# Kernel tuning notes

Hardware: AMD Instinct MI355X
Metric: run time of the kernel (lower is better)

The kernel has to match this reference:

```python
import jax, jax.numpy as jnp
import numpy as np

ROPE_BASE = 10000.0

def rope_tables(n, r):
    inv = 1.0 / (ROPE_BASE ** (jnp.arange(0, r, 2, dtype=jnp.float32) / r))  # [r/2]
    ang = jnp.arange(n, dtype=jnp.float32)[:, None] * inv[None, :]           # [n, r/2]
    cos = jnp.concatenate([jnp.cos(ang), jnp.cos(ang)], axis=-1)             # [n, r]
    sin = jnp.concatenate([jnp.sin(ang), jnp.sin(ang)], axis=-1)
    return cos, sin

def apply_rope(x, cos, sin):
    # x: [B, H, T, r]; cos/sin: [T, r]
    half = x.shape[-1] // 2
    x_rot = jnp.concatenate([-x[..., half:], x[..., :half]], axis=-1)
    return x * cos + x_rot * sin

def setup_inputs() -> dict:
    key = jax.random.key(0)
    ks = jax.random.split(key, 8)
    B, S, L = 2, 1024, 1024
    dim_q, h, k, d_c, d_cq, r = 2048, 16, 128, 512, 1536, 64
    w = 0.02  # weight scale to keep activations numerically tame
    return {
        'hidden_q': jax.random.normal(ks[0], (B, S, dim_q), jnp.float32),
        'kv_c':     jax.random.normal(ks[1], (B, L, d_c), jnp.float32),
        'Wq':       jax.random.normal(ks[2], (h * k, dim_q), jnp.float32) * w,
        'w_kc_q':   jax.random.normal(ks[3], (h, k, d_cq), jnp.float32) * w,
        'W_qr':     jax.random.normal(ks[4], (h, d_cq, r), jnp.float32) * (w / np.sqrt(r)),
        'W_kr':     jax.random.normal(ks[5], (h, d_c, r), jnp.float32) * w,
        'w_kc_kv':  jax.random.normal(ks[6], (h, k, d_c), jnp.float32) * w,
        'Wo':       jax.random.normal(ks[7], (dim_q, h * k), jnp.float32) * w,
    }

def reference(hidden_q, kv_c, Wq, w_kc_q, W_qr, W_kr, w_kc_kv, Wo):
    B, S, _ = hidden_q.shape
    L = kv_c.shape[1]
    h, k, _ = w_kc_q.shape
    r = W_qr.shape[-1]
    # q projection: [B,S,h,k]
    q_hk = (hidden_q @ Wq.T).reshape(B, S, h, k)
    # low-rank expand to q-compressed space then retrieval space
    q_big = jnp.einsum('bshk,hkq->bshq', q_hk, w_kc_q)          # [B,S,h,d_cq]
    q_r = jnp.einsum('bshq,hqr->bhsr', q_big, W_qr)             # [B,h,S,r]
    k_r = jnp.einsum('bld,hdr->bhlr', kv_c, W_kr)               # [B,h,L,r]
    cos_S, sin_S = rope_tables(S, r)
    cos_L, sin_L = rope_tables(L, r)
    q_r = apply_rope(q_r, cos_S, sin_S)
    k_r = apply_rope(k_r, cos_L, sin_L)
    # attention in retrieval space, values are compressed kv (shared across heads)
    scores = jnp.einsum('bhsr,bhlr->bhsl', q_r, k_r)            # scale baked into W_qr
    attn = jax.nn.softmax(scores, axis=-1)
    ctx_c = jnp.einsum('bhsl,bld->bhsd', attn, kv_c)            # [B,h,S,d_c]
    # decompress per head: w_kc_kv is [h,k,d_c]
    ctx_lat = jnp.einsum('bhsd,hkd->bshk', ctx_c, w_kc_kv).reshape(B, S, h * k)
    return ctx_lat @ Wo.T
```

## Files before the change

kernel.cpp:

```cpp
#include <hip/hip_runtime.h>
#include <math.h>
#include <stdint.h>


typedef __attribute__((ext_vector_type(8))) short short8;
typedef __attribute__((ext_vector_type(4))) float f32x4;

#define GLOAD16(gsrc, ldst)                                                            \
  __builtin_amdgcn_global_load_lds((const __attribute__((address_space(1))) void*)(gsrc), \
                                   (__attribute__((address_space(3))) void*)(ldst), 16, 0, 0)

__device__ inline uint16_t f2b(float x) {
  uint32_t u = __builtin_bit_cast(uint32_t, x);
  u += 0x7fff + ((u >> 16) & 1);
  return (uint16_t)(u >> 16);
}
__device__ inline float b2f(uint16_t b) {
  uint32_t u = ((uint32_t)b) << 16;
  return __builtin_bit_cast(float, u);
}
__device__ inline uint32_t cvtpk_bf16(float lo, float hi) {
  uint32_t d;
  asm("v_cvt_pk_bf16_f32 %0, %1, %2" : "=v"(d) : "v"(lo), "v"(hi));
  return d;
}

__global__ __launch_bounds__(256) void convert5_kernel(
    const float* __restrict__ s0, uint16_t* __restrict__ t0, const float* __restrict__ s1,
    uint16_t* __restrict__ t1, const float* __restrict__ s2, uint16_t* __restrict__ t2,
    const float* __restrict__ s3, uint16_t* __restrict__ t3, const float* __restrict__ s4,
    uint16_t* __restrict__ t4) {
  int bid = blockIdx.x;
  const float* s;
  uint16_t* t;
  int off;
  if (bid < 2048) { s = s0; t = t0; off = bid; }
  else if (bid < 2560) { s = s1; t = t1; off = bid - 2048; }
  else if (bid < 3072) { s = s2; t = t2; off = bid - 2560; }
  else if (bid < 5120) { s = s3; t = t3; off = bid - 3072; }
  else { s = s4; t = t4; off = bid - 5120; }
  int i = off * 256 + threadIdx.x;
  const float4* s4v = (const float4*)s;
  float4 a = s4v[i * 2], b = s4v[i * 2 + 1];
  union {
    uint16_t u[8];
    uint4 v;
  } o;
  o.u[0] = f2b(a.x); o.u[1] = f2b(a.y); o.u[2] = f2b(a.z); o.u[3] = f2b(a.w);
  o.u[4] = f2b(b.x); o.u[5] = f2b(b.y); o.u[6] = f2b(b.z); o.u[7] = f2b(b.w);
  ((uint4*)t)[i] = o.v;
}

__global__ __launch_bounds__(256) void transpose_conv_kernel(const float* __restrict__ src,
                                                             uint16_t* __restrict__ dst,
                                                             int R, int C, int sOff, int dOff) {
  __shared__ float t[32][33];
  src += (size_t)blockIdx.z * sOff;
  dst += (size_t)blockIdx.z * dOff;
  int r0 = blockIdx.x * 32, c0 = blockIdx.y * 32;
  int tr = threadIdx.x >> 5, tc = threadIdx.x & 31;
#pragma unroll
  for (int i = 0; i < 4; ++i) t[tr + i * 8][tc] = src[(size_t)(r0 + tr + i * 8) * C + c0 + tc];
  __syncthreads();
#pragma unroll
  for (int i = 0; i < 4; ++i)
    dst[(size_t)(c0 + tr + i * 8) * R + r0 + tc] = f2b(t[tc][tr + i * 8]);
}

__global__ __launch_bounds__(64) void rope_tables_kernel(float* __restrict__ cosK,
                                                         float* __restrict__ sinK,
                                                         float* __restrict__ cosQ,
                                                         float* __restrict__ sinQ) {
  const float LOG2E = 1.44269504088896341f;
  int s = blockIdx.x;
  int j = threadIdx.x;
  int i = j & 31;
  float inv = powf(10000.0f, -(float)(2 * i) / 64.0f);
  float ang = (float)s * inv;
  float c = cosf(ang), sn = sinf(ang);
  cosK[s * 64 + j] = c;
  sinK[s * 64 + j] = sn;
  cosQ[s * 64 + j] = c * LOG2E;
  sinQ[s * 64 + j] = sn * LOG2E;
}

template <int BM, int EPI, int SPLITK = 1>
__global__ __launch_bounds__(256) void gemm_mfma_kernel(const uint16_t* __restrict__ A,
                                                        const uint16_t* __restrict__ Bt,
                                                        void* __restrict__ Cv, int K, int lda,
                                                        int ldb, int ldc, int aZ, int bZ, int cZ,
                                                        const float* __restrict__ rc,
                                                        const float* __restrict__ rs) {
  constexpr int MT = BM / 32;
  __shared__ __align__(16) uint16_t As[2][BM * 64];
  __shared__ __align__(16) uint16_t Bs[2][128 * 64];
  int z = blockIdx.z;
  if (SPLITK > 1) {
    int zh = z / SPLITK, zk = z % SPLITK;
    A += (size_t)zh * aZ + (size_t)zk * K;
    Bt += (size_t)zh * bZ + (size_t)zk * K;
  } else {
    A += (size_t)z * aZ;
    Bt += (size_t)z * bZ;
  }
  int m0 = blockIdx.x * BM, n0 = blockIdx.y * 128;
  int tid = threadIdx.x;
  int wave = tid >> 6, lane = tid & 63;
  int wm = wave >> 1, wn = wave & 1;
  int rS = lane >> 3, sl = lane & 7;
  int lr = lane >> 4, lc = lane & 15;

  auto stage = [&](int k0, int buf) {
#pragma unroll
    for (int i = 0; i < MT; ++i) {
      int idx = wave * MT + i;
      int row = idx * 8 + rS;
      GLOAD16(A + (size_t)(m0 + row) * lda + k0 + ((sl ^ (row & 7)) << 3),
              (uint8_t*)As[buf] + idx * 1024);
    }
#pragma unroll
    for (int i = 0; i < 4; ++i) {
      int idx = wave * 4 + i;
      int row = idx * 8 + rS;
      GLOAD16(Bt + (size_t)(n0 + row) * ldb + k0 + ((sl ^ (row & 7)) << 3),
              (uint8_t*)Bs[buf] + idx * 1024);
    }
  };

  f32x4 acc[MT][4] = {};
  stage(0, 0);
  int cur = 0;
  for (int k0 = 0; k0 < K; k0 += 64) {
    __syncthreads();
    if (k0 + 64 < K) stage(k0 + 64, cur ^ 1);
    short8 af[MT][2], bf[4][2];
#pragma unroll
    for (int t = 0; t < MT; ++t)
#pragma unroll
      for (int ks = 0; ks < 2; ++ks) {
        int slot = ks * 4 + lr;
        int ra = wm * (BM / 2) + t * 16 + lc;
        af[t][ks] =
            *(const short8*)((const uint8_t*)As[cur] + ra * 128 + ((slot ^ (ra & 7)) << 4));
      }
#pragma unroll
    for (int t = 0; t < 4; ++t)
#pragma unroll
      for (int ks = 0; ks < 2; ++ks) {
        int slot = ks * 4 + lr;
        int rb = wn * 64 + t * 16 + lc;
        bf[t][ks] =
            *(const short8*)((const uint8_t*)Bs[cur] + rb * 128 + ((slot ^ (rb & 7)) << 4));
      }
    __builtin_amdgcn_s_setprio(1);
#pragma unroll
    for (int mt = 0; mt < MT; ++mt)
#pragma unroll
      for (int nt = 0; nt < 4; ++nt) {
        acc[mt][nt] =
            __builtin_amdgcn_mfma_f32_16x16x32_bf16(af[mt][0], bf[nt][0], acc[mt][nt], 0, 0, 0);
        acc[mt][nt] =
            __builtin_amdgcn_mfma_f32_16x16x32_bf16(af[mt][1], bf[nt][1], acc[mt][nt], 0, 0, 0);
      }
    __builtin_amdgcn_s_setprio(0);
    cur ^= 1;
  }
  if (EPI == 3) {
#pragma unroll
    for (int mt = 0; mt < MT; ++mt)
#pragma unroll
      for (int nt = 0; nt < 4; ++nt)
#pragma unroll
        for (int r = 0; r < 4; ++r) {
          int m = m0 + wm * (BM / 2) + mt * 16 + lr * 4 + r;
          int n = n0 + wn * 64 + nt * 16 + lc;
          int pos = m & 1023, j = n & 63;
          float x = acc[mt][nt][r];
          float prt = acc[mt][nt ^ 2][r];
          float rot = (nt & 2) ? prt : -prt;
          float v = fmaf(x, rc[pos * 64 + j], rot * rs[pos * 64 + j]);
          ((uint16_t*)Cv)[(size_t)m * ldc + n] = f2b(v);
        }
  } else {
#pragma unroll
    for (int mt = 0; mt < MT; ++mt)
#pragma unroll
      for (int nt = 0; nt < 4; ++nt)
#pragma unroll
        for (int r = 0; r < 4; ++r) {
          int m = m0 + wm * (BM / 2) + mt * 16 + lr * 4 + r;
          int n = n0 + wn * 64 + nt * 16 + lc;
          float v = acc[mt][nt][r];
          if (EPI == 0)
            ((float*)Cv)[(size_t)z * cZ + (size_t)m * ldc + n] = v;
          else if (EPI == 1)
            ((uint16_t*)Cv)[(size_t)z * cZ + (size_t)m * ldc + n] = f2b(v);
          else
            ((uint16_t*)Cv)[((size_t)((m >> 10) * 2048 + n)) * 1024 + (m & 1023)] = f2b(v);
        }
  }
}

__global__ __launch_bounds__(256) void reduce1_kernel(const float* __restrict__ tp,
                                                      uint16_t* __restrict__ tmpT) {
  int gid = blockIdx.x * 256 + threadIdx.x;
  int zh = gid >> 13, e = gid & 8191;
  const float* b = tp + (size_t)zh * 32768 + e;
  tmpT[gid] = f2b(b[0] + b[8192] + b[16384] + b[24576]);
}

__global__ __launch_bounds__(512, 4) void flash3_kernel(const uint16_t* __restrict__ qrb,
                                                        const uint16_t* __restrict__ krb,
                                                        const uint16_t* __restrict__ VhT,
                                                        uint16_t* __restrict__ ctxlatb) {
  __shared__ __align__(16) uint8_t lds[67584];
  int bh = blockIdx.x;
  int b = bh >> 4, h = bh & 15;
  int s0 = blockIdx.y * 64;
  int tid = threadIdx.x, wave = tid >> 6, lane = tid & 63;
  int ig = wave >> 2, w = wave & 3;
  int lr = lane >> 4, lc = lane & 15;
  int rS = lane >> 3, sl = lane & 7;

  uint8_t* Ks = lds + ig * 8192;
  uint8_t* Vs = lds + 16384 + ig * 16384;
  uint8_t* Ps = lds + 49152 + wave * 2304;

  const uint16_t* qrow = qrb + (size_t)(b * 1024 + s0 + w * 16 + lc) * 1024 + h * 64;
  short8 qa[2];
  qa[0] = *(const short8*)(qrow + lr * 8);
  qa[1] = *(const short8*)(qrow + 32 + lr * 8);

  float m_run = -1e30f, l_run = 0.f;
  f32x4 o[8] = {};

  uint8_t* psW = Ps + lc * 144 + lr * 8;
  const uint8_t* psR = Ps + lc * 144 + lr * 16;

  const uint16_t* krbase = krb + (size_t)(b * 1024) * 1024 + h * 64;
  const uint16_t* vtbase = VhT + (size_t)(b * 2048 + h * 128) * 1024;

  auto stageKV = [&](int l0) {
#pragma unroll
    for (int i = 0; i < 2; ++i) {
      int idx = w * 2 + i;
      int row = idx * 8 + rS;
      GLOAD16(krbase + (size_t)(l0 + row) * 1024 + ((sl ^ (row & 7)) << 3), Ks + idx * 1024);
    }
#pragma unroll
    for (int i = 0; i < 4; ++i) {
      int idx = w * 4 + i;
      int row = idx * 8 + rS;
      GLOAD16(vtbase + (size_t)row * 1024 + l0 + ((sl ^ (row & 7)) << 3), Vs + idx * 1024);
    }
  };

  for (int t = 0; t < 8; ++t) {
    int l0 = ig * 512 + t * 64;
    __syncthreads();
    stageKV(l0);
    __syncthreads();

    f32x4 sc[4];
    __builtin_amdgcn_s_setprio(1);
#pragma unroll
    for (int nt = 0; nt < 4; ++nt) {
      int rowk = nt * 16 + lc;
      short8 kb0 = *(const short8*)(Ks + rowk * 128 + ((lr ^ (rowk & 7)) << 4));
      short8 kb1 = *(const short8*)(Ks + rowk * 128 + (((4 + lr) ^ (rowk & 7)) << 4));
      f32x4 z = {};
      z = __builtin_amdgcn_mfma_f32_16x16x32_bf16(kb0, qa[0], z, 0, 0, 0);
      sc[nt] = __builtin_amdgcn_mfma_f32_16x16x32_bf16(kb1, qa[1], z, 0, 0, 0);
    }
    __builtin_amdgcn_s_setprio(0);

    float mx = fmaxf(fmaxf(fmaxf(sc[0][0], sc[0][1]), fmaxf(sc[0][2], sc[0][3])),
                     fmaxf(fmaxf(sc[1][0], sc[1][1]), fmaxf(sc[1][2], sc[1][3])));
    float mx2 = fmaxf(fmaxf(fmaxf(sc[2][0], sc[2][1]), fmaxf(sc[2][2], sc[2][3])),
                      fmaxf(fmaxf(sc[3][0], sc[3][1]), fmaxf(sc[3][2], sc[3][3])));
    mx = fmaxf(mx, mx2);
    mx = fmaxf(mx, __shfl_xor(mx, 16));
    mx = fmaxf(mx, __shfl_xor(mx, 32));

    bool grow = mx > m_run + 8.0f;
    bool upd = (__ballot(grow) != 0ULL);
    float scale;
    if (upd) {
      float mn = fmaxf(m_run, mx);
      scale = exp2f(m_run - mn);
      m_run = mn;
    }

    float ps = 0.f;
#pragma unroll
    for (int nt = 0; nt < 4; ++nt) {
#pragma unroll
      for (int rp = 0; rp < 2; ++rp) {
        float p0 = exp2f(sc[nt][rp * 2] - m_run);
        float p1 = exp2f(sc[nt][rp * 2 + 1] - m_run);
        ps += p0 + p1;
        *(uint32_t*)(psW + nt * 32 + rp * 4) = cvtpk_bf16(p0, p1);
      }
    }
    ps += __shfl_xor(ps, 16);
    ps += __shfl_xor(ps, 32);

    if (upd) {
      l_run = l_run * scale + ps;
      float sc0 = __shfl(scale, lr * 4 + 0);
      float sc1 = __shfl(scale, lr * 4 + 1);
      float sc2 = __shfl(scale, lr * 4 + 2);
      float sc3 = __shfl(scale, lr * 4 + 3);
#pragma unroll
      for (int nt = 0; nt < 8; ++nt) {
        o[nt][0] *= sc0;
        o[nt][1] *= sc1;
        o[nt][2] *= sc2;
        o[nt][3] *= sc3;
      }
    } else {
      l_run += ps;
    }

    short8 pa[2];
    pa[0] = *(const short8*)(psR);
    pa[1] = *(const short8*)(psR + 64);
    __builtin_amdgcn_s_setprio(1);
#pragma unroll
    for (int nt = 0; nt < 8; ++nt) {
      int rowv = nt * 16 + lc;
      short8 vb0 = *(const short8*)(Vs + rowv * 128 + ((lr ^ (rowv & 7)) << 4));
      short8 vb1 = *(const short8*)(Vs + rowv * 128 + (((4 + lr) ^ (rowv & 7)) << 4));
      o[nt] = __builtin_amdgcn_mfma_f32_16x16x32_bf16(pa[0], vb0, o[nt], 0, 0, 0);
      o[nt] = __builtin_amdgcn_mfma_f32_16x16x32_bf16(pa[1], vb1, o[nt], 0, 0, 0);
    }
    __builtin_amdgcn_s_setprio(0);
  }

  __syncthreads();
  float2* mlx = (float2*)(lds + 49152);
  if (lr == 0) mlx[(ig * 4 + w) * 16 + lc] = make_float2(m_run, l_run);
  __syncthreads();
  float2 e0 = mlx[(0 * 4 + w) * 16 + lc];
  float2 e1 = mlx[(1 * 4 + w) * 16 + lc];
  float M = fmaxf(e0.x, e1.x);
  float a0 = exp2f(e0.x - M), a1 = exp2f(e1.x - M);
  float dinv = 1.0f / (e0.y * a0 + e1.y * a1);
  float myA = ig ? a1 : a0;
  float ar[4], dr[4];
#pragma unroll
  for (int r = 0; r < 4; ++r) {
    ar[r] = __shfl(myA, lr * 4 + r);
    dr[r] = __shfl(dinv, lr * 4 + r);
  }
  float* O1 = (float*)lds;
  int qb = w * 16 + lr * 4;
  if (ig == 1) {
#pragma unroll
    for (int nt = 0; nt < 8; ++nt)
#pragma unroll
      for (int r = 0; r < 4; ++r) O1[(qb + r) * 130 + nt * 16 + lc] = o[nt][r] * ar[r];
  }
  __syncthreads();
  if (ig == 0) {
    uint16_t* orow = ctxlatb + (size_t)(b * 1024 + s0 + w * 16) * 2048 + h * 128;
#pragma unroll
    for (int nt = 0; nt < 8; ++nt)
#pragma unroll
      for (int r = 0; r < 4; ++r) {
        float v = (o[nt][r] * ar[r] + O1[(qb + r) * 130 + nt * 16 + lc]) * dr[r];
        orow[(size_t)(lr * 4 + r) * 2048 + nt * 16 + lc] = f2b(v);
      }
  }
}

extern "C" void kernel_launch(void* const* d_in, const int* in_sizes, int n_in,
                              void* d_out, int out_size, void* d_ws, size_t ws_size,
                              hipStream_t stream) {
  const float* hidden_q = (const float*)d_in[0];
  const float* kv_c = (const float*)d_in[1];
  const float* Wq = (const float*)d_in[2];
  const float* w_kc_q = (const float*)d_in[3];
  const float* W_qr = (const float*)d_in[4];
  const float* W_kr = (const float*)d_in[5];
  const float* w_kc_kv = (const float*)d_in[6];
  const float* Wo = (const float*)d_in[7];
  float* out = (float*)d_out;

  const size_t MB = 1024 * 1024;
  uint8_t* base = (uint8_t*)d_ws;
  uint16_t* Wob = (uint16_t*)(base + 0 * MB);
  uint16_t* qrb = (uint16_t*)(base + 8 * MB);
  uint16_t* krb = (uint16_t*)(base + 12 * MB);
  uint16_t* VhT = (uint16_t*)(base + 16 * MB);
  uint16_t* ctxlatb = (uint16_t*)(base + 24 * MB);
  float* cosK = (float*)(base + 32 * MB);
  float* sinK = (float*)(base + 32 * MB + 262144);
  float* cosQ = (float*)(base + 32 * MB + 524288);
  float* sinQ = (float*)(base + 32 * MB + 786432);
  uint16_t* hqb = (uint16_t*)(base + 33 * MB);
  uint16_t* kvb = (uint16_t*)(base + 41 * MB);
  uint16_t* wkvb = (uint16_t*)(base + 43 * MB);
  uint16_t* WqT = (uint16_t*)(base + 45 * MB);
  uint16_t* WqrT = (uint16_t*)(base + 53 * MB);
  uint16_t* wkcqb = (uint16_t*)(base + 56 * MB);
  float* tmp1 = (float*)(base + 62 * MB);
  uint16_t* tmpT = (uint16_t*)(base + 64 * MB);
  uint16_t* WkrT = (uint16_t*)(base + 64 * MB + 262144);

  convert5_kernel<<<dim3(6656), dim3(256), 0, stream>>>(hidden_q, hqb, kv_c, kvb, w_kc_kv, wkvb,
                                                        Wo, Wob, w_kc_q, wkcqb);
  rope_tables_kernel<<<dim3(1024), dim3(64), 0, stream>>>(cosK, sinK, cosQ, sinQ);
  transpose_conv_kernel<<<dim3(48, 2, 16), dim3(256), 0, stream>>>((const float*)W_qr, WqrT, 1536,
                                                                   64, 98304, 98304);
  transpose_conv_kernel<<<dim3(64, 64, 1), dim3(256), 0, stream>>>(Wq, WqT, 2048, 2048, 0, 0);
  transpose_conv_kernel<<<dim3(16, 2, 16), dim3(256), 0, stream>>>((const float*)W_kr, WkrT, 512,
                                                                   64, 32768, 32768);
  gemm_mfma_kernel<64, 0, 4><<<dim3(1, 1, 64), dim3(256), 0, stream>>>(
      WqrT, wkcqb, tmp1, 384, 1536, 1536, 128, 98304, 196608, 8192, nullptr, nullptr);
  reduce1_kernel<<<dim3(512), dim3(256), 0, stream>>>(tmp1, tmpT);
  uint16_t* WfoldT = wkcqb;
  gemm_mfma_kernel<64, 1><<<dim3(1, 16, 16), dim3(256), 0, stream>>>(
      tmpT, WqT, WfoldT, 128, 128, 2048, 2048, 8192, 128, 131072, nullptr, nullptr);
  gemm_mfma_kernel<64, 3><<<dim3(32, 8), dim3(256), 0, stream>>>(hqb, WfoldT, qrb, 2048, 2048,
                                                                 2048, 1024, 0, 0, 0, cosQ, sinQ);
  gemm_mfma_kernel<64, 3><<<dim3(32, 8), dim3(256), 0, stream>>>(kvb, WkrT, krb, 512, 512, 512,
                                                                 1024, 0, 0, 0, cosK, sinK);
  gemm_mfma_kernel<64, 2><<<dim3(32, 16), dim3(256), 0, stream>>>(kvb, wkvb, VhT, 512, 512, 512, 0,
                                                                  0, 0, 0, nullptr, nullptr);
  flash3_kernel<<<dim3(32, 16), dim3(512), 0, stream>>>(qrb, krb, VhT, ctxlatb);
  gemm_mfma_kernel<64, 0><<<dim3(32, 16), dim3(256), 0, stream>>>(ctxlatb, Wob, out, 2048, 2048,
                                                                  2048, 2048, 0, 0, 0, nullptr,
                                                                  nullptr);
}
```

Baseline: 151.0 us.

## Merge prep launches and use larger M tiles for V and output GEMMs

```diff
diff --git a/kernel.cpp b/kernel.cpp
--- a/kernel.cpp
+++ b/kernel.cpp
@@ -29,8 +29,23 @@
     const float* __restrict__ s0, uint16_t* __restrict__ t0, const float* __restrict__ s1,
     uint16_t* __restrict__ t1, const float* __restrict__ s2, uint16_t* __restrict__ t2,
     const float* __restrict__ s3, uint16_t* __restrict__ t3, const float* __restrict__ s4,
-    uint16_t* __restrict__ t4) {
+    uint16_t* __restrict__ t4, float* __restrict__ cosK, float* __restrict__ sinK,
+    float* __restrict__ cosQ, float* __restrict__ sinQ) {
   int bid = blockIdx.x;
+  if (bid >= 6656) {
+    const float LOG2E = 1.44269504088896341f;
+    int idx = (bid - 6656) * 256 + threadIdx.x;
+    int s = idx >> 6, j = idx & 63;
+    int i = j & 31;
+    float inv = powf(10000.0f, -(float)(2 * i) / 64.0f);
+    float ang = (float)s * inv;
+    float c = cosf(ang), sn = sinf(ang);
+    cosK[idx] = c;
+    sinK[idx] = sn;
+    cosQ[idx] = c * LOG2E;
+    sinQ[idx] = sn * LOG2E;
+    return;
+  }
   const float* s;
   uint16_t* t;
   int off;
@@ -51,13 +66,30 @@
   ((uint4*)t)[i] = o.v;
 }
 
-__global__ __launch_bounds__(256) void transpose_conv_kernel(const float* __restrict__ src,
-                                                             uint16_t* __restrict__ dst,
-                                                             int R, int C, int sOff, int dOff) {
+__global__ __launch_bounds__(256) void transpose3_kernel(
+    const float* __restrict__ Wq, uint16_t* __restrict__ WqT, const float* __restrict__ W_qr,
+    uint16_t* __restrict__ WqrT, const float* __restrict__ W_kr, uint16_t* __restrict__ WkrT) {
   __shared__ float t[32][33];
-  src += (size_t)blockIdx.z * sOff;
-  dst += (size_t)blockIdx.z * dOff;
-  int r0 = blockIdx.x * 32, c0 = blockIdx.y * 32;
+  int bid = blockIdx.x;
+  const float* src;
+  uint16_t* dst;
+  int R, C, r0, c0;
+  if (bid < 4096) {
+    src = Wq; dst = WqT; R = 2048; C = 2048;
+    r0 = (bid & 63) * 32; c0 = (bid >> 6) * 32;
+  } else if (bid < 5632) {
+    int b = bid - 4096;
+    int z = b / 96, rem = b % 96;
+    src = W_qr + (size_t)z * 98304; dst = WqrT + (size_t)z * 98304;
+    R = 1536; C = 64;
+    r0 = (rem >> 1) * 32; c0 = (rem & 1) * 32;
+  } else {
+    int b = bid - 5632;
+    int z = b / 32, rem = b % 32;
+    src = W_kr + (size_t)z * 32768; dst = WkrT + (size_t)z * 32768;
+    R = 512; C = 64;
+    r0 = (rem >> 1) * 32; c0 = (rem & 1) * 32;
+  }
   int tr = threadIdx.x >> 5, tc = threadIdx.x & 31;
 #pragma unroll
   for (int i = 0; i < 4; ++i) t[tr + i * 8][tc] = src[(size_t)(r0 + tr + i * 8) * C + c0 + tc];
@@ -65,23 +97,6 @@
 #pragma unroll
   for (int i = 0; i < 4; ++i)
     dst[(size_t)(c0 + tr + i * 8) * R + r0 + tc] = f2b(t[tc][tr + i * 8]);
-}
-
-__global__ __launch_bounds__(64) void rope_tables_kernel(float* __restrict__ cosK,
-                                                         float* __restrict__ sinK,
-                                                         float* __restrict__ cosQ,
-                                                         float* __restrict__ sinQ) {
-  const float LOG2E = 1.44269504088896341f;
-  int s = blockIdx.x;
-  int j = threadIdx.x;
-  int i = j & 31;
-  float inv = powf(10000.0f, -(float)(2 * i) / 64.0f);
-  float ang = (float)s * inv;
-  float c = cosf(ang), sn = sinf(ang);
-  cosK[s * 64 + j] = c;
-  sinK[s * 64 + j] = sn;
-  cosQ[s * 64 + j] = c * LOG2E;
-  sinQ[s * 64 + j] = sn * LOG2E;
 }
 
 template <int BM, int EPI, int SPLITK = 1>
@@ -408,14 +423,11 @@
   uint16_t* tmpT = (uint16_t*)(base + 64 * MB);
   uint16_t* WkrT = (uint16_t*)(base + 64 * MB + 262144);
 
-  convert5_kernel<<<dim3(6656), dim3(256), 0, stream>>>(hidden_q, hqb, kv_c, kvb, w_kc_kv, wkvb,
-                                                        Wo, Wob, w_kc_q, wkcqb);
-  rope_tables_kernel<<<dim3(1024), dim3(64), 0, stream>>>(cosK, sinK, cosQ, sinQ);
-  transpose_conv_kernel<<<dim3(48, 2, 16), dim3(256), 0, stream>>>((const float*)W_qr, WqrT, 1536,
-                                                                   64, 98304, 98304);
-  transpose_conv_kernel<<<dim3(64, 64, 1), dim3(256), 0, stream>>>(Wq, WqT, 2048, 2048, 0, 0);
-  transpose_conv_kernel<<<dim3(16, 2, 16), dim3(256), 0, stream>>>((const float*)W_kr, WkrT, 512,
-                                                                   64, 32768, 32768);
+  convert5_kernel<<<dim3(6912), dim3(256), 0, stream>>>(hidden_q, hqb, kv_c, kvb, w_kc_kv, wkvb,
+                                                        Wo, Wob, w_kc_q, wkcqb, cosK, sinK, cosQ,
+                                                        sinQ);
+  transpose3_kernel<<<dim3(6144), dim3(256), 0, stream>>>(Wq, WqT, (const float*)W_qr, WqrT,
+                                                          (const float*)W_kr, WkrT);
   gemm_mfma_kernel<64, 0, 4><<<dim3(1, 1, 64), dim3(256), 0, stream>>>(
       WqrT, wkcqb, tmp1, 384, 1536, 1536, 128, 98304, 196608, 8192, nullptr, nullptr);
   reduce1_kernel<<<dim3(512), dim3(256), 0, stream>>>(tmp1, tmpT);
@@ -426,10 +438,10 @@
                                                                  2048, 1024, 0, 0, 0, cosQ, sinQ);
   gemm_mfma_kernel<64, 3><<<dim3(32, 8), dim3(256), 0, stream>>>(kvb, WkrT, krb, 512, 512, 512,
                                                                  1024, 0, 0, 0, cosK, sinK);
-  gemm_mfma_kernel<64, 2><<<dim3(32, 16), dim3(256), 0, stream>>>(kvb, wkvb, VhT, 512, 512, 512, 0,
-                                                                  0, 0, 0, nullptr, nullptr);
+  gemm_mfma_kernel<128, 2><<<dim3(16, 16), dim3(256), 0, stream>>>(kvb, wkvb, VhT, 512, 512, 512,
+                                                                   0, 0, 0, 0, nullptr, nullptr);
   flash3_kernel<<<dim3(32, 16), dim3(512), 0, stream>>>(qrb, krb, VhT, ctxlatb);
-  gemm_mfma_kernel<64, 0><<<dim3(32, 16), dim3(256), 0, stream>>>(ctxlatb, Wob, out, 2048, 2048,
-                                                                  2048, 2048, 0, 0, 0, nullptr,
-                                                                  nullptr);
-}
+  gemm_mfma_kernel<128, 0><<<dim3(16, 16), dim3(256), 0, stream>>>(ctxlatb, Wob, out, 2048, 2048,
+                                                                   2048, 2048, 0, 0, 0, nullptr,
+                                                                   nullptr);
+}
```

New measurement: 154.2 us. 1.02x slower.
